# Kernel optimization log

Hardware: AMD Instinct MI355X
Metric: run time of the kernel (lower is better)

Reference implementation:

```python
import jax, jax.numpy as jnp
import numpy as np
import math

EMB_DIM = 1024
HEAD_SIZE = 64
T = 4096
B = 4

def setup_inputs() -> dict:
    key = jax.random.key(0)
    k1, k2, k3, k4 = jax.random.split(key, 4)
    scale = 1.0 / math.sqrt(EMB_DIM)
    return {
        "input": jax.random.normal(k1, (B, T, EMB_DIM), dtype=jnp.float32),
        "Wq": jax.random.normal(k2, (EMB_DIM, HEAD_SIZE), dtype=jnp.float32) * scale,
        "Wk": jax.random.normal(k3, (EMB_DIM, HEAD_SIZE), dtype=jnp.float32) * scale,
        "Wv": jax.random.normal(k4, (EMB_DIM, HEAD_SIZE), dtype=jnp.float32) * scale,
    }

def reference(input, Wq, Wk, Wv):
    # q,k,v: [B,T,H]
    q = input @ Wq
    k = input @ Wk
    v = input @ Wv
    # scores: [B,T,T]
    match = jnp.einsum('bqh,bkh->bqk', q, k)
    # 'encoder' mask in this repo = causal tril mask
    causal = jnp.tril(jnp.ones((T, T), dtype=bool))
    match = jnp.where(causal, match, -jnp.inf)
    # NOTE: faithful to source quirk: softmax first, THEN divide by sqrt(head_size)
    attention = jax.nn.softmax(match, axis=-1) / math.sqrt(HEAD_SIZE)
    return jnp.einsum('bqk,bkh->bqh', attention, v)
```

## Files before the change

### kernel.cpp

```cpp
#include <hip/hip_runtime.h>

#define T_SEQ 4096
#define NBATCH 4
#define EMB 1024
#define HS 64
#define BT (NBATCH * T_SEQ)

typedef float f32x4 __attribute__((ext_vector_type(4)));
typedef short s16x8 __attribute__((ext_vector_type(8)));

__device__ __forceinline__ unsigned short f2bf(float x) {
  union { float f; unsigned u; } c; c.f = x;
  unsigned r = c.u + 0x7FFF + ((c.u >> 16) & 1);
  return (unsigned short)(r >> 16);
}
__device__ __forceinline__ float bf2f(unsigned short h) {
  union { unsigned u; float f; } c; c.u = ((unsigned)h) << 16;
  return c.f;
}
__device__ __forceinline__ void cvt8(float4 a0, float4 a1, s16x8& hi, s16x8& lo) {
  float xv[8] = {a0.x, a0.y, a0.z, a0.w, a1.x, a1.y, a1.z, a1.w};
#pragma unroll
  for (int j = 0; j < 8; ++j) {
    unsigned short h = f2bf(xv[j]);
    hi[j] = (short)h;
    lo[j] = (short)f2bf(xv[j] - bf2f(h));
  }
}

__global__ __launch_bounds__(256) void wconv(
    const float* __restrict__ Wq, const float* __restrict__ Wk,
    const float* __restrict__ Wv, unsigned short* __restrict__ wt_hi,
    unsigned short* __restrict__ wt_lo) {
  const int n3 = blockIdx.x;
  const int which = n3 >> 6, n = n3 & 63;
  const float* W = (which == 0) ? Wq : (which == 1) ? Wk : Wv;
#pragma unroll
  for (int i = 0; i < 4; ++i) {
    int k = i * 256 + threadIdx.x;
    float x = W[(size_t)k * HS + n];
    unsigned short h = f2bf(x);
    wt_hi[(size_t)n3 * EMB + k] = h;
    wt_lo[(size_t)n3 * EMB + k] = f2bf(x - bf2f(h));
  }
}

__global__ __launch_bounds__(512) void qkv_mfma(
    const float* __restrict__ inp, const unsigned short* __restrict__ wt_hi,
    const unsigned short* __restrict__ wt_lo, float* __restrict__ qf,
    unsigned short* __restrict__ khi, unsigned short* __restrict__ klo,
    unsigned short* __restrict__ vtb) {
  __shared__ unsigned short Bhi[192 * 72];
  __shared__ unsigned short Blo[192 * 72];
  const int t = threadIdx.x, lane = t & 63, w = t >> 6;
  const int m = lane & 15, quad = lane >> 4;
  const int mg = w >> 1, ng = w & 1;
  const int tok0 = blockIdx.x * 64;
  const int arow = tok0 + mg * 16 + m;

  f32x4 acc[6];
#pragma unroll
  for (int nt = 0; nt < 6; ++nt) acc[nt] = (f32x4){0.f, 0.f, 0.f, 0.f};

  const int s0 = t, s1 = t + 512, s2 = t + 1024;
  const int n3_0 = s0 >> 3, k8_0 = s0 & 7;
  const int n3_1 = s1 >> 3, k8_1 = s1 & 7;
  const int n3_2 = s2 >> 3, k8_2 = s2 & 7;
  const size_t goff0 = (size_t)n3_0 * EMB + k8_0 * 8;
  const size_t goff1 = (size_t)n3_1 * EMB + k8_1 * 8;
  const size_t goff2 = (size_t)n3_2 * EMB + k8_2 * 8;
  const int lds0 = n3_0 * 72 + k8_0 * 8;
  const int lds1 = n3_1 * 72 + k8_1 * 8;
  const int lds2 = n3_2 * 72 + k8_2 * 8;

  uint4 ph0, ph1, ph2, pl0, pl1, pl2;
  float4 pa0, pa1, pa2, pa3;
  ph0 = *(const uint4*)&wt_hi[goff0];
  ph1 = *(const uint4*)&wt_hi[goff1];
  ph2 = *(const uint4*)&wt_hi[goff2];
  pl0 = *(const uint4*)&wt_lo[goff0];
  pl1 = *(const uint4*)&wt_lo[goff1];
  pl2 = *(const uint4*)&wt_lo[goff2];
  {
    const float* ap = &inp[(size_t)arow * EMB + quad * 8];
    pa0 = *(const float4*)ap;
    pa1 = *(const float4*)(ap + 4);
    pa2 = *(const float4*)(ap + 32);
    pa3 = *(const float4*)(ap + 36);
  }

  for (int kc = 0; kc < 16; ++kc) {
    __syncthreads();
    *(uint4*)&Bhi[lds0] = ph0;
    *(uint4*)&Bhi[lds1] = ph1;
    *(uint4*)&Bhi[lds2] = ph2;
    *(uint4*)&Blo[lds0] = pl0;
    *(uint4*)&Blo[lds1] = pl1;
    *(uint4*)&Blo[lds2] = pl2;
    __syncthreads();

    s16x8 ah0, al0, ah1, al1;
    cvt8(pa0, pa1, ah0, al0);
    cvt8(pa2, pa3, ah1, al1);

    if (kc < 15) {
      const int k0n = (kc + 1) * 64;
      ph0 = *(const uint4*)&wt_hi[goff0 + k0n];
      ph1 = *(const uint4*)&wt_hi[goff1 + k0n];
      ph2 = *(const uint4*)&wt_hi[goff2 + k0n];
      pl0 = *(const uint4*)&wt_lo[goff0 + k0n];
      pl1 = *(const uint4*)&wt_lo[goff1 + k0n];
      pl2 = *(const uint4*)&wt_lo[goff2 + k0n];
      const float* ap = &inp[(size_t)arow * EMB + k0n + quad * 8];
      pa0 = *(const float4*)ap;
      pa1 = *(const float4*)(ap + 4);
      pa2 = *(const float4*)(ap + 32);
      pa3 = *(const float4*)(ap + 36);
    }

#pragma unroll
    for (int nt = 0; nt < 6; ++nt) {
      const int n3 = ng * 96 + nt * 16 + m;
      s16x8 bh0 = *(const s16x8*)&Bhi[n3 * 72 + quad * 8];
      s16x8 bl0 = *(const s16x8*)&Blo[n3 * 72 + quad * 8];
      s16x8 bh1 = *(const s16x8*)&Bhi[n3 * 72 + 32 + quad * 8];
      s16x8 bl1 = *(const s16x8*)&Blo[n3 * 72 + 32 + quad * 8];
      acc[nt] = __builtin_amdgcn_mfma_f32_16x16x32_bf16(ah0, bh0, acc[nt], 0, 0, 0);
      acc[nt] = __builtin_amdgcn_mfma_f32_16x16x32_bf16(ah0, bl0, acc[nt], 0, 0, 0);
      acc[nt] = __builtin_amdgcn_mfma_f32_16x16x32_bf16(al0, bh0, acc[nt], 0, 0, 0);
      acc[nt] = __builtin_amdgcn_mfma_f32_16x16x32_bf16(ah1, bh1, acc[nt], 0, 0, 0);
      acc[nt] = __builtin_amdgcn_mfma_f32_16x16x32_bf16(ah1, bl1, acc[nt], 0, 0, 0);
      acc[nt] = __builtin_amdgcn_mfma_f32_16x16x32_bf16(al1, bh1, acc[nt], 0, 0, 0);
    }
  }

#pragma unroll
  for (int nt = 0; nt < 6; ++nt) {
    int n3 = ng * 96 + nt * 16 + m;
    int which = n3 >> 6, col = n3 & 63;
#pragma unroll
    for (int r = 0; r < 4; ++r) {
      int tok = tok0 + mg * 16 + quad * 4 + r;
      float val = acc[nt][r];
      if (which == 0) {
        qf[(size_t)tok * HS + col] = val;
      } else if (which == 1) {
        unsigned short h = f2bf(val);
        khi[(size_t)tok * HS + col] = h;
        klo[(size_t)tok * HS + col] = f2bf(val - bf2f(h));
      } else {
        vtb[(size_t)(tok >> 6) * 4096 + (size_t)col * 64 + (tok & 63)] = f2bf(val);
      }
    }
  }
}

__global__ __launch_bounds__(256) void attn_part(
    const float* __restrict__ q, const unsigned short* __restrict__ khi,
    const unsigned short* __restrict__ klo, const unsigned short* __restrict__ vt,
    unsigned short* __restrict__ partO, float* __restrict__ partML) {
  __shared__ unsigned short Khi_s[64 * 72];
  __shared__ unsigned short Klo_s[64 * 72];
  __shared__ unsigned short Vt_s[64 * 72];
  __shared__ unsigned short P_s[4 * 16 * 72];
  const int t = threadIdx.x;
  const int lane = t & 63, w = t >> 6;
  const int m = lane & 15, quad = lane >> 4;

  int u = blockIdx.x;
  const int b = u / 160;
  u -= b * 160;
  int qtile = 0, c = 0;
  {
    int acc2 = 0;
    for (int qq = 0; qq < 64; ++qq) {
      int ncq = (qq >> 4) + 1;
      if (u < acc2 + ncq) { qtile = qq; c = u - acc2; break; }
      acc2 += ncq;
    }
  }
  const int kt0 = c * 16;
  const int kt1 = (kt0 + 16 < qtile + 1) ? kt0 + 16 : qtile + 1;

  const size_t qrow0 = (size_t)b * T_SEQ + (size_t)qtile * 64;
  const size_t krowbase = (size_t)b * T_SEQ;
  const int q_loc = w * 16 + m;

  s16x8 qh[2], ql[2];
#pragma unroll
  for (int cc = 0; cc < 2; ++cc) {
    const float* qp = &q[(qrow0 + q_loc) * HS + cc * 32 + quad * 8];
    cvt8(*(const float4*)qp, *(const float4*)(qp + 4), qh[cc], ql[cc]);
  }

  float l_st = 0.f;
  f32x4 o[4];
#pragma unroll
  for (int hb = 0; hb < 4; ++hb) o[hb] = (f32x4){0.f, 0.f, 0.f, 0.f};

  const int r0 = t >> 3, ch0 = t & 7;
  const int r1 = (256 + t) >> 3, ch1 = t & 7;

  uint4 pk0h, pk0l, pv0, pk1h, pk1l, pv1;
  {
    size_t g0 = (krowbase + (size_t)kt0 * 64 + r0) * HS + ch0 * 8;
    size_t g1 = (krowbase + (size_t)kt0 * 64 + r1) * HS + ch1 * 8;
    pk0h = *(const uint4*)&khi[g0]; pk0l = *(const uint4*)&klo[g0];
    pk1h = *(const uint4*)&khi[g1]; pk1l = *(const uint4*)&klo[g1];
    size_t v0 = (size_t)(b * 64 + kt0) * 4096 + (size_t)r0 * 64 + ch0 * 8;
    size_t v1 = (size_t)(b * 64 + kt0) * 4096 + (size_t)r1 * 64 + ch1 * 8;
    pv0 = *(const uint4*)&vt[v0]; pv1 = *(const uint4*)&vt[v1];
  }

  for (int kt = kt0; kt < kt1; ++kt) {
    __syncthreads();
    *(uint4*)&Khi_s[r0 * 72 + ch0 * 8] = pk0h;
    *(uint4*)&Klo_s[r0 * 72 + ch0 * 8] = pk0l;
    *(uint4*)&Vt_s[r0 * 72 + ch0 * 8] = pv0;
    *(uint4*)&Khi_s[r1 * 72 + ch1 * 8] = pk1h;
    *(uint4*)&Klo_s[r1 * 72 + ch1 * 8] = pk1l;
    *(uint4*)&Vt_s[r1 * 72 + ch1 * 8] = pv1;
    __syncthreads();

    if (kt + 1 < kt1) {
      size_t g0 = (krowbase + (size_t)(kt + 1) * 64 + r0) * HS + ch0 * 8;
      size_t g1 = (krowbase + (size_t)(kt + 1) * 64 + r1) * HS + ch1 * 8;
      pk0h = *(const uint4*)&khi[g0]; pk0l = *(const uint4*)&klo[g0];
      pk1h = *(const uint4*)&khi[g1]; pk1l = *(const uint4*)&klo[g1];
      size_t v0 = (size_t)(b * 64 + kt + 1) * 4096 + (size_t)r0 * 64 + ch0 * 8;
      size_t v1 = (size_t)(b * 64 + kt + 1) * 4096 + (size_t)r1 * 64 + ch1 * 8;
      pv0 = *(const uint4*)&vt[v0]; pv1 = *(const uint4*)&vt[v1];
    }

    f32x4 st[4];
#pragma unroll
    for (int cb = 0; cb < 4; ++cb) {
      st[cb] = (f32x4){0.f, 0.f, 0.f, 0.f};
#pragma unroll
      for (int cc = 0; cc < 2; ++cc) {
        s16x8 bh = *(const s16x8*)&Khi_s[(cb * 16 + m) * 72 + cc * 32 + quad * 8];
        s16x8 bl = *(const s16x8*)&Klo_s[(cb * 16 + m) * 72 + cc * 32 + quad * 8];
        st[cb] = __builtin_amdgcn_mfma_f32_16x16x32_bf16(bh, qh[cc], st[cb], 0, 0, 0);
        st[cb] = __builtin_amdgcn_mfma_f32_16x16x32_bf16(bl, qh[cc], st[cb], 0, 0, 0);
        st[cb] = __builtin_amdgcn_mfma_f32_16x16x32_bf16(bh, ql[cc], st[cb], 0, 0, 0);
      }
    }
    if (kt == qtile) {
#pragma unroll
      for (int cb = 0; cb < 4; ++cb)
#pragma unroll
        for (int r = 0; r < 4; ++r)
          if (cb * 16 + quad * 4 + r > q_loc) st[cb][r] = -1e30f;
    }
#pragma unroll
    for (int cb = 0; cb < 4; ++cb)
#pragma unroll
      for (int r = 0; r < 4; ++r) {
        st[cb][r] = __expf(st[cb][r]);
        l_st += st[cb][r];
      }
#pragma unroll
    for (int cb = 0; cb < 4; ++cb) {
      uint2 pk;
      pk.x = (unsigned)f2bf(st[cb][0]) | ((unsigned)f2bf(st[cb][1]) << 16);
      pk.y = (unsigned)f2bf(st[cb][2]) | ((unsigned)f2bf(st[cb][3]) << 16);
      *(uint2*)&P_s[q_loc * 72 + cb * 16 + quad * 4] = pk;
    }
    s16x8 pf[2];
#pragma unroll
    for (int cc = 0; cc < 2; ++cc)
      pf[cc] = *(const s16x8*)&P_s[q_loc * 72 + cc * 32 + quad * 8];
#pragma unroll
    for (int hb = 0; hb < 4; ++hb) {
#pragma unroll
      for (int cc = 0; cc < 2; ++cc) {
        s16x8 vf = *(const s16x8*)&Vt_s[(hb * 16 + m) * 72 + cc * 32 + quad * 8];
        o[hb] = __builtin_amdgcn_mfma_f32_16x16x32_bf16(vf, pf[cc], o[hb], 0, 0, 0);
      }
    }
  }

  l_st += __shfl_xor(l_st, 16, 64);
  l_st += __shfl_xor(l_st, 32, 64);

  const int slot = ((b * 64 + qtile) << 2) + c;
  unsigned short* Op = partO + (size_t)slot * 4096;
#pragma unroll
  for (int hb = 0; hb < 4; ++hb) {
    uint2 pk;
    pk.x = (unsigned)f2bf(o[hb][0]) | ((unsigned)f2bf(o[hb][1]) << 16);
    pk.y = (unsigned)f2bf(o[hb][2]) | ((unsigned)f2bf(o[hb][3]) << 16);
    *(uint2*)&Op[q_loc * 64 + hb * 16 + quad * 4] = pk;
  }
  if (quad == 0) partML[(size_t)slot * 64 + q_loc] = l_st;
}

__global__ __launch_bounds__(256) void attn_combine(
    const unsigned short* __restrict__ partO, const float* __restrict__ partML,
    float* __restrict__ out) {
  const int qtile = blockIdx.x, b = blockIdx.y;
  const int t = threadIdx.x;
  const int row = t >> 2, hg = t & 3;
  const int nc = (qtile >> 4) + 1;
  const int slot0 = (b * 64 + qtile) << 2;

  float lsum = 0.f;
  for (int i = 0; i < nc; ++i) lsum += partML[(size_t)(slot0 + i) * 64 + row];
  const float inv = 1.f / (lsum * 8.0f);

  float acc[16];
#pragma unroll
  for (int e = 0; e < 16; ++e) acc[e] = 0.f;
  for (int i = 0; i < nc; ++i) {
    const unsigned short* Op =
        partO + (size_t)(slot0 + i) * 4096 + row * 64 + hg * 16;
    uint4 u0 = *(const uint4*)Op;
    uint4 u1 = *(const uint4*)(Op + 8);
    unsigned uv[8] = {u0.x, u0.y, u0.z, u0.w, u1.x, u1.y, u1.z, u1.w};
#pragma unroll
    for (int e = 0; e < 8; ++e) {
      acc[2 * e] += bf2f((unsigned short)(uv[e] & 0xFFFF));
      acc[2 * e + 1] += bf2f((unsigned short)(uv[e] >> 16));
    }
  }
  float* op = &out[((size_t)b * T_SEQ + (size_t)qtile * 64 + row) * HS + hg * 16];
#pragma unroll
  for (int v = 0; v < 4; ++v) {
    float4 r;
    r.x = acc[4 * v + 0] * inv; r.y = acc[4 * v + 1] * inv;
    r.z = acc[4 * v + 2] * inv; r.w = acc[4 * v + 3] * inv;
    ((float4*)op)[v] = r;
  }
}

extern "C" void kernel_launch(void* const* d_in, const int* in_sizes, int n_in,
                              void* d_out, int out_size, void* d_ws, size_t ws_size,
                              hipStream_t stream) {
  const float* inp = (const float*)d_in[0];
  const float* Wq  = (const float*)d_in[1];
  const float* Wk  = (const float*)d_in[2];
  const float* Wv  = (const float*)d_in[3];
  float* out = (float*)d_out;

  char* base = (char*)d_ws;
  float* qf = (float*)base;
  unsigned short* khi = (unsigned short*)(base + (size_t)BT * HS * 4);
  unsigned short* klo = khi + (size_t)BT * HS;
  unsigned short* vtb = klo + (size_t)BT * HS;
  unsigned short* wt_hi = vtb + (size_t)BT * HS;
  unsigned short* wt_lo = wt_hi + (size_t)192 * EMB;
  unsigned short* partO = wt_lo + (size_t)192 * EMB;
  float* partML = (float*)(partO + (size_t)1024 * 4096);

  wconv<<<dim3(192), dim3(256), 0, stream>>>(Wq, Wk, Wv, wt_hi, wt_lo);
  qkv_mfma<<<dim3(BT / 64), dim3(512), 0, stream>>>(inp, wt_hi, wt_lo, qf, khi, klo, vtb);
  attn_part<<<dim3(640), dim3(256), 0, stream>>>(qf, khi, klo, vtb, partO, partML);
  attn_combine<<<dim3(64, NBATCH), dim3(256), 0, stream>>>(partO, partML, out);
}
```

Before: 173.2 us.

## Split QKV projection columns across two blocks and widen the K step

The QKV projection kernel now launches twice as many blocks, each computing half of the 192 output columns (96) for a 64-token tile. The K chunk per iteration doubles to 128, so there are half as many loop iterations and barriers, with a wider padded LDS tile. It also sets an occupancy hint in the launch bounds. This raises parallelism and cuts per-iteration sync overhead, but each input row is now read and converted to bf16 twice, once by each of the two blocks.

New measurement: 253.5 us. 46.4% more time.

```diff
diff --git a/kernel.cpp b/kernel.cpp
--- a/kernel.cpp
+++ b/kernel.cpp
@@ -45,36 +45,39 @@
   }
 }
 
-__global__ __launch_bounds__(512) void qkv_mfma(
+__global__ __launch_bounds__(512, 4) void qkv_mfma(
     const float* __restrict__ inp, const unsigned short* __restrict__ wt_hi,
     const unsigned short* __restrict__ wt_lo, float* __restrict__ qf,
     unsigned short* __restrict__ khi, unsigned short* __restrict__ klo,
     unsigned short* __restrict__ vtb) {
-  __shared__ unsigned short Bhi[192 * 72];
-  __shared__ unsigned short Blo[192 * 72];
+  __shared__ unsigned short Bhi[96 * 136];
+  __shared__ unsigned short Blo[96 * 136];
   const int t = threadIdx.x, lane = t & 63, w = t >> 6;
   const int m = lane & 15, quad = lane >> 4;
   const int mg = w >> 1, ng = w & 1;
-  const int tok0 = blockIdx.x * 64;
+  const int rc = blockIdx.x >> 1;
+  const int half = blockIdx.x & 1;
+  const int tok0 = rc * 64;
   const int arow = tok0 + mg * 16 + m;
-
-  f32x4 acc[6];
-#pragma unroll
-  for (int nt = 0; nt < 6; ++nt) acc[nt] = (f32x4){0.f, 0.f, 0.f, 0.f};
+  const int colbase = half * 96;
+
+  f32x4 acc[3];
+#pragma unroll
+  for (int nt = 0; nt < 3; ++nt) acc[nt] = (f32x4){0.f, 0.f, 0.f, 0.f};
 
   const int s0 = t, s1 = t + 512, s2 = t + 1024;
-  const int n3_0 = s0 >> 3, k8_0 = s0 & 7;
-  const int n3_1 = s1 >> 3, k8_1 = s1 & 7;
-  const int n3_2 = s2 >> 3, k8_2 = s2 & 7;
-  const size_t goff0 = (size_t)n3_0 * EMB + k8_0 * 8;
-  const size_t goff1 = (size_t)n3_1 * EMB + k8_1 * 8;
-  const size_t goff2 = (size_t)n3_2 * EMB + k8_2 * 8;
-  const int lds0 = n3_0 * 72 + k8_0 * 8;
-  const int lds1 = n3_1 * 72 + k8_1 * 8;
-  const int lds2 = n3_2 * 72 + k8_2 * 8;
+  const int n3_0 = s0 >> 4, k8_0 = s0 & 15;
+  const int n3_1 = s1 >> 4, k8_1 = s1 & 15;
+  const int n3_2 = s2 >> 4, k8_2 = s2 & 15;
+  const size_t goff0 = (size_t)(colbase + n3_0) * EMB + k8_0 * 8;
+  const size_t goff1 = (size_t)(colbase + n3_1) * EMB + k8_1 * 8;
+  const size_t goff2 = (size_t)(colbase + n3_2) * EMB + k8_2 * 8;
+  const int lds0 = n3_0 * 136 + k8_0 * 8;
+  const int lds1 = n3_1 * 136 + k8_1 * 8;
+  const int lds2 = n3_2 * 136 + k8_2 * 8;
 
   uint4 ph0, ph1, ph2, pl0, pl1, pl2;
-  float4 pa0, pa1, pa2, pa3;
+  float4 pa0, pa1, pa2, pa3, pa4, pa5, pa6, pa7;
   ph0 = *(const uint4*)&wt_hi[goff0];
   ph1 = *(const uint4*)&wt_hi[goff1];
   ph2 = *(const uint4*)&wt_hi[goff2];
@@ -83,13 +86,13 @@
   pl2 = *(const uint4*)&wt_lo[goff2];
   {
     const float* ap = &inp[(size_t)arow * EMB + quad * 8];
-    pa0 = *(const float4*)ap;
-    pa1 = *(const float4*)(ap + 4);
-    pa2 = *(const float4*)(ap + 32);
-    pa3 = *(const float4*)(ap + 36);
-  }
-
-  for (int kc = 0; kc < 16; ++kc) {
+    pa0 = *(const float4*)ap;        pa1 = *(const float4*)(ap + 4);
+    pa2 = *(const float4*)(ap + 32); pa3 = *(const float4*)(ap + 36);
+    pa4 = *(const float4*)(ap + 64); pa5 = *(const float4*)(ap + 68);
+    pa6 = *(const float4*)(ap + 96); pa7 = *(const float4*)(ap + 100);
+  }
+
+  for (int kc = 0; kc < 8; ++kc) {
     __syncthreads();
     *(uint4*)&Bhi[lds0] = ph0;
     *(uint4*)&Bhi[lds1] = ph1;
@@ -99,12 +102,14 @@
     *(uint4*)&Blo[lds2] = pl2;
     __syncthreads();
 
-    s16x8 ah0, al0, ah1, al1;
+    s16x8 ah0, al0, ah1, al1, ah2, al2, ah3, al3;
     cvt8(pa0, pa1, ah0, al0);
     cvt8(pa2, pa3, ah1, al1);
-
-    if (kc < 15) {
-      const int k0n = (kc + 1) * 64;
+    cvt8(pa4, pa5, ah2, al2);
+    cvt8(pa6, pa7, ah3, al3);
+
+    if (kc < 7) {
+      const int k0n = (kc + 1) * 128;
       ph0 = *(const uint4*)&wt_hi[goff0 + k0n];
       ph1 = *(const uint4*)&wt_hi[goff1 + k0n];
       ph2 = *(const uint4*)&wt_hi[goff2 + k0n];
@@ -112,31 +117,37 @@
       pl1 = *(const uint4*)&wt_lo[goff1 + k0n];
       pl2 = *(const uint4*)&wt_lo[goff2 + k0n];
       const float* ap = &inp[(size_t)arow * EMB + k0n + quad * 8];
-      pa0 = *(const float4*)ap;
-      pa1 = *(const float4*)(ap + 4);
-      pa2 = *(const float4*)(ap + 32);
-      pa3 = *(const float4*)(ap + 36);
-    }
-
-#pragma unroll
-    for (int nt = 0; nt < 6; ++nt) {
-      const int n3 = ng * 96 + nt * 16 + m;
-      s16x8 bh0 = *(const s16x8*)&Bhi[n3 * 72 + quad * 8];
-      s16x8 bl0 = *(const s16x8*)&Blo[n3 * 72 + quad * 8];
-      s16x8 bh1 = *(const s16x8*)&Bhi[n3 * 72 + 32 + quad * 8];
-      s16x8 bl1 = *(const s16x8*)&Blo[n3 * 72 + 32 + quad * 8];
-      acc[nt] = __builtin_amdgcn_mfma_f32_16x16x32_bf16(ah0, bh0, acc[nt], 0, 0, 0);
-      acc[nt] = __builtin_amdgcn_mfma_f32_16x16x32_bf16(ah0, bl0, acc[nt], 0, 0, 0);
-      acc[nt] = __builtin_amdgcn_mfma_f32_16x16x32_bf16(al0, bh0, acc[nt], 0, 0, 0);
-      acc[nt] = __builtin_amdgcn_mfma_f32_16x16x32_bf16(ah1, bh1, acc[nt], 0, 0, 0);
-      acc[nt] = __builtin_amdgcn_mfma_f32_16x16x32_bf16(ah1, bl1, acc[nt], 0, 0, 0);
-      acc[nt] = __builtin_amdgcn_mfma_f32_16x16x32_bf16(al1, bh1, acc[nt], 0, 0, 0);
-    }
-  }
-
-#pragma unroll
-  for (int nt = 0; nt < 6; ++nt) {
-    int n3 = ng * 96 + nt * 16 + m;
+      pa0 = *(const float4*)ap;        pa1 = *(const float4*)(ap + 4);
+      pa2 = *(const float4*)(ap + 32); pa3 = *(const float4*)(ap + 36);
+      pa4 = *(const float4*)(ap + 64); pa5 = *(const float4*)(ap + 68);
+      pa6 = *(const float4*)(ap + 96); pa7 = *(const float4*)(ap + 100);
+    }
+
+#define MFMA3(AH, AL, CCOFF, A)                                              \
+    {                                                                        \
+      s16x8 bh = *(const s16x8*)&Bhi[bbase + (CCOFF) + quad * 8];            \
+      s16x8 bl = *(const s16x8*)&Blo[bbase + (CCOFF) + quad * 8];            \
+      A = __builtin_amdgcn_mfma_f32_16x16x32_bf16(AH, bh, A, 0, 0, 0);       \
+      A = __builtin_amdgcn_mfma_f32_16x16x32_bf16(AH, bl, A, 0, 0, 0);       \
+      A = __builtin_amdgcn_mfma_f32_16x16x32_bf16(AL, bh, A, 0, 0, 0);       \
+    }
+
+#pragma unroll
+    for (int nt = 0; nt < 3; ++nt) {
+      const int bbase = (ng * 48 + nt * 16 + m) * 136;
+      f32x4 a = acc[nt];
+      MFMA3(ah0, al0, 0, a);
+      MFMA3(ah1, al1, 32, a);
+      MFMA3(ah2, al2, 64, a);
+      MFMA3(ah3, al3, 96, a);
+      acc[nt] = a;
+    }
+#undef MFMA3
+  }
+
+#pragma unroll
+  for (int nt = 0; nt < 3; ++nt) {
+    int n3 = colbase + ng * 48 + nt * 16 + m;
     int which = n3 >> 6, col = n3 & 63;
 #pragma unroll
     for (int r = 0; r < 4; ++r) {
@@ -353,7 +364,7 @@
   float* partML = (float*)(partO + (size_t)1024 * 4096);
 
   wconv<<<dim3(192), dim3(256), 0, stream>>>(Wq, Wk, Wv, wt_hi, wt_lo);
-  qkv_mfma<<<dim3(BT / 64), dim3(512), 0, stream>>>(inp, wt_hi, wt_lo, qf, khi, klo, vtb);
+  qkv_mfma<<<dim3(BT / 64 * 2), dim3(512), 0, stream>>>(inp, wt_hi, wt_lo, qf, khi, klo, vtb);
   attn_part<<<dim3(640), dim3(256), 0, stream>>>(qf, khi, klo, vtb, partO, partML);
   attn_combine<<<dim3(64, NBATCH), dim3(256), 0, stream>>>(partO, partML, out);
 }
```

## Double-buffer QKV projection weights in LDS and truncate activation split

Applied to the files above, without the earlier changes.

Restructures the QKV projection GEMM loop to ping-pong between two LDS buffers. This cuts the barrier count to one per k-chunk and lets global loads for the next chunks overlap the MFMA work. It also replaces the round-to-nearest bf16 hi/lo split of the fp32 input with a cheaper truncation-based split packed two values per word. The extra LDS doubles shared memory per block, which may lower occupancy, and the truncated hi part shifts some precision into the lo term.

Result: faster. 168.5 us (-2.7%).

```diff
diff --git a/kernel.cpp b/kernel.cpp
--- a/kernel.cpp
+++ b/kernel.cpp
@@ -26,6 +26,25 @@
     hi[j] = (short)h;
     lo[j] = (short)f2bf(xv[j] - bf2f(h));
   }
+}
+__device__ __forceinline__ void cvt8t(float4 a0, float4 a1, s16x8& hi, s16x8& lo) {
+  float xv[8] = {a0.x, a0.y, a0.z, a0.w, a1.x, a1.y, a1.z, a1.w};
+  unsigned hu[8], lu[8];
+#pragma unroll
+  for (int j = 0; j < 8; ++j) {
+    union { float f; unsigned u; } c; c.f = xv[j];
+    hu[j] = c.u;
+    union { unsigned u; float f; } hf; hf.u = c.u & 0xFFFF0000u;
+    union { float f; unsigned u; } r; r.f = xv[j] - hf.f;
+    lu[j] = r.u;
+  }
+  union { s16x8 v; unsigned u[4]; } H, L;
+#pragma unroll
+  for (int j = 0; j < 4; ++j) {
+    H.u[j] = (hu[2 * j] >> 16) | (hu[2 * j + 1] & 0xFFFF0000u);
+    L.u[j] = (lu[2 * j] >> 16) | (lu[2 * j + 1] & 0xFFFF0000u);
+  }
+  hi = H.v; lo = L.v;
 }
 
 __global__ __launch_bounds__(256) void wconv(
@@ -50,8 +69,10 @@
     const unsigned short* __restrict__ wt_lo, float* __restrict__ qf,
     unsigned short* __restrict__ khi, unsigned short* __restrict__ klo,
     unsigned short* __restrict__ vtb) {
-  __shared__ unsigned short Bhi[192 * 72];
-  __shared__ unsigned short Blo[192 * 72];
+  __shared__ unsigned short Bh0[192 * 72];
+  __shared__ unsigned short Bl0[192 * 72];
+  __shared__ unsigned short Bh1[192 * 72];
+  __shared__ unsigned short Bl1[192 * 72];
   const int t = threadIdx.x, lane = t & 63, w = t >> 6;
   const int m = lane & 15, quad = lane >> 4;
   const int mg = w >> 1, ng = w & 1;
@@ -73,66 +94,98 @@
   const int lds1 = n3_1 * 72 + k8_1 * 8;
   const int lds2 = n3_2 * 72 + k8_2 * 8;
 
-  uint4 ph0, ph1, ph2, pl0, pl1, pl2;
-  float4 pa0, pa1, pa2, pa3;
-  ph0 = *(const uint4*)&wt_hi[goff0];
-  ph1 = *(const uint4*)&wt_hi[goff1];
-  ph2 = *(const uint4*)&wt_hi[goff2];
-  pl0 = *(const uint4*)&wt_lo[goff0];
-  pl1 = *(const uint4*)&wt_lo[goff1];
-  pl2 = *(const uint4*)&wt_lo[goff2];
-  {
-    const float* ap = &inp[(size_t)arow * EMB + quad * 8];
-    pa0 = *(const float4*)ap;
-    pa1 = *(const float4*)(ap + 4);
-    pa2 = *(const float4*)(ap + 32);
-    pa3 = *(const float4*)(ap + 36);
-  }
-
-  for (int kc = 0; kc < 16; ++kc) {
+#define LOAD_B(K0, PH0, PH1, PH2, PL0, PL1, PL2)            \
+  PH0 = *(const uint4*)&wt_hi[goff0 + (K0)];                \
+  PH1 = *(const uint4*)&wt_hi[goff1 + (K0)];                \
+  PH2 = *(const uint4*)&wt_hi[goff2 + (K0)];                \
+  PL0 = *(const uint4*)&wt_lo[goff0 + (K0)];                \
+  PL1 = *(const uint4*)&wt_lo[goff1 + (K0)];                \
+  PL2 = *(const uint4*)&wt_lo[goff2 + (K0)];
+
+#define STORE_B(BH, BL, PH0, PH1, PH2, PL0, PL1, PL2)       \
+  *(uint4*)&BH[lds0] = PH0;                                 \
+  *(uint4*)&BH[lds1] = PH1;                                 \
+  *(uint4*)&BH[lds2] = PH2;                                 \
+  *(uint4*)&BL[lds0] = PL0;                                 \
+  *(uint4*)&BL[lds1] = PL1;                                 \
+  *(uint4*)&BL[lds2] = PL2;
+
+#define LOAD_A(K0, PA0, PA1, PA2, PA3)                      \
+  {                                                         \
+    const float* ap = &inp[(size_t)arow * EMB + (K0) + quad * 8]; \
+    PA0 = *(const float4*)ap;                               \
+    PA1 = *(const float4*)(ap + 4);                         \
+    PA2 = *(const float4*)(ap + 32);                        \
+    PA3 = *(const float4*)(ap + 36);                        \
+  }
+
+#define QKV_TILE(BH, BL, AH0, AL0, AH1, AL1)                                 \
+  {                                                                          \
+    _Pragma("unroll")                                                        \
+    for (int nt = 0; nt < 6; ++nt) {                                         \
+      const int bbase = (ng * 96 + nt * 16 + m) * 72;                        \
+      f32x4 a = acc[nt];                                                     \
+      {                                                                      \
+        s16x8 bh = *(const s16x8*)&BH[bbase + quad * 8];                     \
+        s16x8 bl = *(const s16x8*)&BL[bbase + quad * 8];                     \
+        a = __builtin_amdgcn_mfma_f32_16x16x32_bf16(AH0, bh, a, 0, 0, 0);    \
+        a = __builtin_amdgcn_mfma_f32_16x16x32_bf16(AH0, bl, a, 0, 0, 0);    \
+        a = __builtin_amdgcn_mfma_f32_16x16x32_bf16(AL0, bh, a, 0, 0, 0);    \
+      }                                                                      \
+      {                                                                      \
+        s16x8 bh = *(const s16x8*)&BH[bbase + 32 + quad * 8];                \
+        s16x8 bl = *(const s16x8*)&BL[bbase + 32 + quad * 8];                \
+        a = __builtin_amdgcn_mfma_f32_16x16x32_bf16(AH1, bh, a, 0, 0, 0);    \
+        a = __builtin_amdgcn_mfma_f32_16x16x32_bf16(AH1, bl, a, 0, 0, 0);    \
+        a = __builtin_amdgcn_mfma_f32_16x16x32_bf16(AL1, bh, a, 0, 0, 0);    \
+      }                                                                      \
+      acc[nt] = a;                                                           \
+    }                                                                        \
+  }
+
+  uint4 phA0, phA1, phA2, plA0, plA1, plA2;
+  uint4 phB0, phB1, phB2, plB0, plB1, plB2;
+  float4 paA0, paA1, paA2, paA3;
+  float4 paB0, paB1, paB2, paB3;
+
+  LOAD_B(0, phA0, phA1, phA2, plA0, plA1, plA2);
+  LOAD_A(0, paA0, paA1, paA2, paA3);
+  STORE_B(Bh0, Bl0, phA0, phA1, phA2, plA0, plA1, plA2);
+  LOAD_B(64, phB0, phB1, phB2, plB0, plB1, plB2);
+  LOAD_A(64, paB0, paB1, paB2, paB3);
+  __syncthreads();
+
+#pragma unroll 1
+  for (int kc = 0; kc < 8; ++kc) {
+    const int kbase = kc * 128;
+    STORE_B(Bh1, Bl1, phB0, phB1, phB2, plB0, plB1, plB2);
+    if (kc < 7) { LOAD_B(kbase + 128, phA0, phA1, phA2, plA0, plA1, plA2); }
+    {
+      s16x8 ah0, al0, ah1, al1;
+      cvt8t(paA0, paA1, ah0, al0);
+      cvt8t(paA2, paA3, ah1, al1);
+      if (kc < 7) { LOAD_A(kbase + 128, paA0, paA1, paA2, paA3); }
+      QKV_TILE(Bh0, Bl0, ah0, al0, ah1, al1);
+    }
     __syncthreads();
-    *(uint4*)&Bhi[lds0] = ph0;
-    *(uint4*)&Bhi[lds1] = ph1;
-    *(uint4*)&Bhi[lds2] = ph2;
-    *(uint4*)&Blo[lds0] = pl0;
-    *(uint4*)&Blo[lds1] = pl1;
-    *(uint4*)&Blo[lds2] = pl2;
-    __syncthreads();
-
-    s16x8 ah0, al0, ah1, al1;
-    cvt8(pa0, pa1, ah0, al0);
-    cvt8(pa2, pa3, ah1, al1);
-
-    if (kc < 15) {
-      const int k0n = (kc + 1) * 64;
-      ph0 = *(const uint4*)&wt_hi[goff0 + k0n];
-      ph1 = *(const uint4*)&wt_hi[goff1 + k0n];
-      ph2 = *(const uint4*)&wt_hi[goff2 + k0n];
-      pl0 = *(const uint4*)&wt_lo[goff0 + k0n];
-      pl1 = *(const uint4*)&wt_lo[goff1 + k0n];
-      pl2 = *(const uint4*)&wt_lo[goff2 + k0n];
-      const float* ap = &inp[(size_t)arow * EMB + k0n + quad * 8];
-      pa0 = *(const float4*)ap;
-      pa1 = *(const float4*)(ap + 4);
-      pa2 = *(const float4*)(ap + 32);
-      pa3 = *(const float4*)(ap + 36);
-    }
-
-#pragma unroll
-    for (int nt = 0; nt < 6; ++nt) {
-      const int n3 = ng * 96 + nt * 16 + m;
-      s16x8 bh0 = *(const s16x8*)&Bhi[n3 * 72 + quad * 8];
-      s16x8 bl0 = *(const s16x8*)&Blo[n3 * 72 + quad * 8];
-      s16x8 bh1 = *(const s16x8*)&Bhi[n3 * 72 + 32 + quad * 8];
-      s16x8 bl1 = *(const s16x8*)&Blo[n3 * 72 + 32 + quad * 8];
-      acc[nt] = __builtin_amdgcn_mfma_f32_16x16x32_bf16(ah0, bh0, acc[nt], 0, 0, 0);
-      acc[nt] = __builtin_amdgcn_mfma_f32_16x16x32_bf16(ah0, bl0, acc[nt], 0, 0, 0);
-      acc[nt] = __builtin_amdgcn_mfma_f32_16x16x32_bf16(al0, bh0, acc[nt], 0, 0, 0);
-      acc[nt] = __builtin_amdgcn_mfma_f32_16x16x32_bf16(ah1, bh1, acc[nt], 0, 0, 0);
-      acc[nt] = __builtin_amdgcn_mfma_f32_16x16x32_bf16(ah1, bl1, acc[nt], 0, 0, 0);
-      acc[nt] = __builtin_amdgcn_mfma_f32_16x16x32_bf16(al1, bh1, acc[nt], 0, 0, 0);
-    }
-  }
+    if (kc < 7) { STORE_B(Bh0, Bl0, phA0, phA1, phA2, plA0, plA1, plA2); }
+    {
+      s16x8 ah0, al0, ah1, al1;
+      cvt8t(paB0, paB1, ah0, al0);
+      cvt8t(paB2, paB3, ah1, al1);
+      if (kc < 7) {
+        LOAD_B(kbase + 192, phB0, phB1, phB2, plB0, plB1, plB2);
+        LOAD_A(kbase + 192, paB0, paB1, paB2, paB3);
+      }
+      QKV_TILE(Bh1, Bl1, ah0, al0, ah1, al1);
+    }
+    if (kc < 7) __syncthreads();
+  }
+
+#undef LOAD_B
+#undef STORE_B
+#undef LOAD_A
+#undef QKV_TILE
 
 #pragma unroll
   for (int nt = 0; nt < 6; ++nt) {
```
